# Kernel optimization log

Hardware: AMD Instinct MI355X
Metric: run time of the kernel (lower is better)

The kernel has to match this reference:

```python
import jax, jax.numpy as jnp
import numpy as np

K = 1024       # vq_codebook_size
DC = 64        # vq_code_dim
BETA = 0.25    # commitment cost
DECAY = 0.99   # EMA decay
EPS = 1e-05


def setup_inputs() -> dict:
    key = jax.random.key(0)
    k1, k2, k3 = jax.random.split(key, 3)
    B, H, W = 32, 64, 64
    return {
        "z_e": jax.random.normal(k1, (B, DC, H, W), dtype=jnp.float32),
        "embedding": jax.random.normal(k2, (K, DC), dtype=jnp.float32),
        "cluster_size": jnp.ones((K,), dtype=jnp.float32),
        "embed_avg": jax.random.normal(k3, (K, DC), dtype=jnp.float32),
    }


def reference(z_e, embedding, cluster_size, embed_avg):
    B, D, H, W = z_e.shape
    # flat: [N, D] detached codes, N = B*H*W
    flat = jax.lax.stop_gradient(z_e).transpose(0, 2, 3, 1).reshape(-1, D).astype(jnp.float32)
    distances = ((flat ** 2).sum(1, keepdims=True)
                 + (embedding ** 2).sum(1)
                 - 2.0 * flat @ embedding.T)
    indices = jnp.argmin(distances, axis=-1)          # [N]
    z_q_flat = embedding[indices]                      # gather [N, D]

    # EMA statistics (training path): one-hot sums via segment_sum (scatter-add)
    counts = jax.ops.segment_sum(jnp.ones_like(indices, dtype=jnp.float32), indices, num_segments=K)
    dw = jax.ops.segment_sum(flat, indices, num_segments=K)  # encodings.T @ flat
    new_cluster_size = cluster_size * DECAY + (1.0 - DECAY) * counts
    new_embed_avg = embed_avg * DECAY + (1.0 - DECAY) * dw
    n = new_cluster_size.sum()
    smoothed = (new_cluster_size + EPS) / (n + K * EPS) * n
    new_embedding = new_embed_avg / smoothed[:, None]

    z_q = z_q_flat.reshape(B, H, W, D).transpose(0, 3, 1, 2)  # [B, D, H, W]
    commitment_loss = BETA * jnp.mean((z_e.astype(jnp.float32) - jax.lax.stop_gradient(z_q)) ** 2)
    # straight-through estimator
    z_q_st = z_e + jax.lax.stop_gradient(z_q.astype(z_e.dtype) - z_e)
    return (z_q_st, indices.reshape(B, H, W), commitment_loss,
            new_embedding, new_cluster_size, new_embed_avg)
```

## Files before the change

kernel.cpp:

```cpp
#include <hip/hip_runtime.h>

#define KCB   1024
#define DCV   64
#define HWN   4096
#define CHW   262144
#define NTOT  131072

#define O_ZQ   0
#define O_IDX  8388608
#define O_LOSS 8519680
#define O_NE   8519681
#define O_NCS  8585217
#define O_NEA  8586241

#define W_LOSS  0
#define W_CTR   64
#define W_E2    256
#define W_HIT   8448
#define W_LOT   139520
#define W_EMBT  270592
#define W_RLIST 532736

#define RCAP   65536
#define MARGIN 0.01f

typedef __attribute__((ext_vector_type(8))) short short8v;
typedef __attribute__((ext_vector_type(4))) float f32x4;

__device__ __forceinline__ unsigned short rne16(float f) {
    unsigned u = __float_as_uint(f);
    unsigned r = (u + 0x7FFFu + ((u >> 16) & 1u)) >> 16;
    return (unsigned short)r;
}

__global__ __launch_bounds__(256) void k_init(
    const float* __restrict__ emb, const float* __restrict__ ea,
    const float* __restrict__ cs, float* __restrict__ out,
    float* __restrict__ e2, short* __restrict__ hiT, short* __restrict__ loT,
    float* __restrict__ embT, double* __restrict__ loss, int* __restrict__ ctr)
{
    int j = blockIdx.x * 256 + threadIdx.x;
    out[O_NEA + j] = 0.99f * ea[j];

    {
        int code = j >> 6, d = j & 63;
        embT[d * KCB + code] = emb[j];
    }
    if (j < KCB) {
        out[O_NCS + j] = 0.99f * cs[j];
        const float* er = emb + j * DCV;
        float s = 0.f;
        #pragma unroll
        for (int d = 0; d < DCV; ++d) { float v = er[d]; s = fmaf(v, v, s); }
        e2[j] = s;
    }
    if (j < 8192) {
        int code = j >> 3, q = j & 7;
        const float* src = emb + code * DCV + q * 8;
        short8v h, l;
        #pragma unroll
        for (int t = 0; t < 8; ++t) {
            float x = src[t];
            unsigned short hb = rne16(x);
            float xh = __uint_as_float(((unsigned)hb) << 16);
            h[t] = (short)hb;
            l[t] = (short)rne16(x - xh);
        }
        *(short8v*)(hiT + (size_t)(q * KCB + code) * 8) = h;
        *(short8v*)(loT + (size_t)(q * KCB + code) * 8) = l;
    }
    if (j == 0) { *loss = 0.0; *ctr = 0; }
}

__global__ __launch_bounds__(256, 2) void k_dist(
    const float* __restrict__ ze, const short* __restrict__ hiT,
    const short* __restrict__ loT, const float* __restrict__ e2g,
    float* __restrict__ out, int* __restrict__ ctr, int* __restrict__ rlist)
{
    __shared__ short ldsH[8 * 128 * 8];
    __shared__ short ldsL[8 * 128 * 8];
    __shared__ float e2s[KCB];

    int tid  = threadIdx.x;
    int lane = tid & 63, w = tid >> 6;
    int g = lane >> 4, c = lane & 15;

    for (int i = tid; i < KCB; i += 256) e2s[i] = e2g[i];

    int rowbase = blockIdx.x * 128 + w * 32;
    short8v ahi[2][2], alo[2][2];
    #pragma unroll
    for (int t = 0; t < 2; ++t) {
        int n = rowbase + t * 16 + c;
        const float* base = ze + (size_t)(n >> 12) * CHW + (n & 4095);
        #pragma unroll
        for (int kh = 0; kh < 2; ++kh) {
            #pragma unroll
            for (int j = 0; j < 8; ++j) {
                int k = kh * 32 + g * 8 + j;
                float x = base[(size_t)k * HWN];
                unsigned short hb = rne16(x);
                float xh = __uint_as_float(((unsigned)hb) << 16);
                ahi[t][kh][j] = (short)hb;
                alo[t][kh][j] = (short)rne16(x - xh);
            }
        }
    }

    float best[8], second[8];
    int   bidx[8];
    #pragma unroll
    for (int i = 0; i < 8; ++i) { best[i] = 3.4e38f; second[i] = 3.4e38f; bidx[i] = 0; }

    for (int ch = 0; ch < 8; ++ch) {
        __syncthreads();
        #pragma unroll
        for (int r = 0; r < 8; ++r) {
            int u = r * 256 + tid;
            int arr = u >> 10;
            int rest = u & 1023;
            int q = rest >> 7, lc = rest & 127;
            const short* s = (arr ? loT : hiT) + (size_t)(q * KCB + ch * 128 + lc) * 8;
            short* d = (arr ? ldsL : ldsH) + rest * 8;
            *(short8v*)d = *(const short8v*)s;
        }
        __syncthreads();

        #pragma unroll 1
        for (int sub = 0; sub < 8; ++sub) {
            int boff = (sub * 16 + c) * 8;
            short8v bh0 = *(const short8v*)&ldsH[(g * 128) * 8 + boff];
            short8v bh1 = *(const short8v*)&ldsH[((4 + g) * 128) * 8 + boff];
            short8v bl0 = *(const short8v*)&ldsL[(g * 128) * 8 + boff];
            short8v bl1 = *(const short8v*)&ldsL[((4 + g) * 128) * 8 + boff];

            f32x4 a0 = {0.f, 0.f, 0.f, 0.f}, a1 = {0.f, 0.f, 0.f, 0.f};
            a0 = __builtin_amdgcn_mfma_f32_16x16x32_bf16(ahi[0][0], bh0, a0, 0, 0, 0);
            a1 = __builtin_amdgcn_mfma_f32_16x16x32_bf16(ahi[1][0], bh0, a1, 0, 0, 0);
            a0 = __builtin_amdgcn_mfma_f32_16x16x32_bf16(ahi[0][1], bh1, a0, 0, 0, 0);
            a1 = __builtin_amdgcn_mfma_f32_16x16x32_bf16(ahi[1][1], bh1, a1, 0, 0, 0);
            a0 = __builtin_amdgcn_mfma_f32_16x16x32_bf16(ahi[0][0], bl0, a0, 0, 0, 0);
            a1 = __builtin_amdgcn_mfma_f32_16x16x32_bf16(ahi[1][0], bl0, a1, 0, 0, 0);
            a0 = __builtin_amdgcn_mfma_f32_16x16x32_bf16(ahi[0][1], bl1, a0, 0, 0, 0);
            a1 = __builtin_amdgcn_mfma_f32_16x16x32_bf16(ahi[1][1], bl1, a1, 0, 0, 0);
            a0 = __builtin_amdgcn_mfma_f32_16x16x32_bf16(alo[0][0], bh0, a0, 0, 0, 0);
            a1 = __builtin_amdgcn_mfma_f32_16x16x32_bf16(alo[1][0], bh0, a1, 0, 0, 0);
            a0 = __builtin_amdgcn_mfma_f32_16x16x32_bf16(alo[0][1], bh1, a0, 0, 0, 0);
            a1 = __builtin_amdgcn_mfma_f32_16x16x32_bf16(alo[1][1], bh1, a1, 0, 0, 0);

            float e2v = e2s[ch * 128 + sub * 16 + c];
            int  code = ch * 128 + sub * 16 + c;
            #pragma unroll
            for (int t = 0; t < 2; ++t) {
                f32x4 av = t ? a1 : a0;
                #pragma unroll
                for (int r = 0; r < 4; ++r) {
                    int i = t * 4 + r;
                    float s = fmaf(-2.f, av[r], e2v);
                    bool lb = s < best[i];
                    float m = lb ? best[i] : s;
                    second[i] = fminf(second[i], m);
                    best[i]   = fminf(best[i], s);
                    bidx[i]   = lb ? code : bidx[i];
                }
            }
        }
    }

    #pragma unroll
    for (int i = 0; i < 8; ++i) {
        float b = best[i], s2 = second[i];
        int bi = bidx[i];
        #pragma unroll
        for (int m = 1; m < 16; m <<= 1) {
            float ob = __shfl_xor(b, m, 64);
            float os = __shfl_xor(s2, m, 64);
            int   oi = __shfl_xor(bi, m, 64);
            float ns = fminf(fmaxf(b, ob), fminf(s2, os));
            bi = (ob < b || (ob == b && oi < bi)) ? oi : bi;
            b  = fminf(b, ob);
            s2 = ns;
        }
        if (c == 0) {
            int t = i >> 2, r = i & 3;
            int n = rowbase + t * 16 + g * 4 + r;
            out[O_IDX + n] = (float)bi;
            if (s2 - b < MARGIN) {
                int p = atomicAdd(ctr, 1);
                if (p < RCAP) rlist[p] = n;
            }
        }
    }
}

__global__ __launch_bounds__(256) void k_refine(
    const float* __restrict__ ze, const float* __restrict__ emb,
    float* __restrict__ out, const int* __restrict__ ctr,
    const int* __restrict__ rlist)
{
    int lane = threadIdx.x & 63;
    int gw   = (blockIdx.x * blockDim.x + threadIdx.x) >> 6;
    int nw   = (gridDim.x * blockDim.x) >> 6;
    int cnt  = *ctr;
    if (cnt > RCAP) cnt = RCAP;

    for (int i = gw; i < cnt; i += nw) {
        int n = rlist[i];
        const float* zp = ze + (size_t)(n >> 12) * CHW + (n & 4095);
        float x[DCV];
        #pragma unroll
        for (int d = 0; d < DCV; ++d) x[d] = zp[(size_t)d * HWN];

        double bd = 1e300;
        int    bi = 0;
        #pragma unroll 1
        for (int cc = 0; cc < KCB / 64; ++cc) {
            int k = cc * 64 + lane;
            const float4* eb4 = (const float4*)(emb + k * DCV);
            double a0 = 0.0, a1 = 0.0;
            #pragma unroll
            for (int q = 0; q < DCV / 4; ++q) {
                float4 v = eb4[q];
                double d0 = (double)x[q * 4 + 0] - (double)v.x;
                double d1 = (double)x[q * 4 + 1] - (double)v.y;
                double d2 = (double)x[q * 4 + 2] - (double)v.z;
                double d3 = (double)x[q * 4 + 3] - (double)v.w;
                a0 = fma(d0, d0, a0); a1 = fma(d1, d1, a1);
                a0 = fma(d2, d2, a0); a1 = fma(d3, d3, a1);
            }
            double dist = a0 + a1;
            if (dist < bd || (dist == bd && k < bi)) { bd = dist; bi = k; }
        }
        #pragma unroll
        for (int off = 32; off > 0; off >>= 1) {
            double od = __shfl_xor(bd, off, 64);
            int    oi = __shfl_xor(bi, off, 64);
            if (od < bd || (od == bd && oi < bi)) { bd = od; bi = oi; }
        }
        if (lane == 0) out[O_IDX + n] = (float)bi;
    }
}

__global__ __launch_bounds__(256) void k_post(
    const float* __restrict__ ze, const float* __restrict__ embT,
    float* __restrict__ out, double* __restrict__ loss)
{
    int gidx = blockIdx.x >> 5, b = blockIdx.x & 31;
    __shared__ float acc[8 * KCB];
    __shared__ float cnt[KCB];
    __shared__ float wsum[4];
    for (int i = threadIdx.x; i < 8 * KCB; i += 256) acc[i] = 0.f;
    if (gidx == 0) for (int i = threadIdx.x; i < KCB; i += 256) cnt[i] = 0.f;
    __syncthreads();

    const float* zp  = ze  + (size_t)b * CHW + (size_t)gidx * 8 * HWN;
    float*       zq  = out + O_ZQ + (size_t)b * CHW + (size_t)gidx * 8 * HWN;
    const float* ipf = out + O_IDX + b * HWN;
    const float* eT  = embT + (size_t)gidx * 8 * KCB;

    float lp = 0.f;
    for (int hw = threadIdx.x; hw < HWN; hw += 256) {
        int idx = (int)ipf[hw];
        #pragma unroll
        for (int i = 0; i < 8; ++i) {
            float x = zp[(size_t)i * HWN + hw];
            float e = eT[i * KCB + idx];
            float df = x - e;
            lp = fmaf(df, df, lp);
            zq[(size_t)i * HWN + hw] = x + (e - x);
            atomicAdd(&acc[idx * 8 + i], x);
        }
        if (gidx == 0) atomicAdd(&cnt[idx], 1.f);
    }

    #pragma unroll
    for (int off = 32; off > 0; off >>= 1) lp += __shfl_down(lp, off, 64);
    int lane = threadIdx.x & 63, wid = threadIdx.x >> 6;
    if (lane == 0) wsum[wid] = lp;
    __syncthreads();
    if (threadIdx.x == 0) {
        double s = (double)wsum[0] + wsum[1] + wsum[2] + wsum[3];
        atomicAdd(loss, s);
    }

    for (int j = threadIdx.x; j < 8192; j += 256) {
        float v = acc[j];
        if (v != 0.f) atomicAdd(&out[O_NEA + (j >> 3) * DCV + gidx * 8 + (j & 7)], 0.01f * v);
    }
    if (gidx == 0)
        for (int k = threadIdx.x; k < KCB; k += 256) {
            float cv = cnt[k];
            if (cv != 0.f) atomicAdd(&out[O_NCS + k], 0.01f * cv);
        }
}

__global__ __launch_bounds__(256) void k_fin(
    float* __restrict__ out, const double* __restrict__ loss)
{
    __shared__ float red[4];
    int t = threadIdx.x;
    float s = 0.f;
    #pragma unroll
    for (int q = 0; q < 4; ++q) s += out[O_NCS + t * 4 + q];
    #pragma unroll
    for (int off = 32; off > 0; off >>= 1) s += __shfl_down(s, off, 64);
    int lane = t & 63, wid = t >> 6;
    if (lane == 0) red[wid] = s;
    __syncthreads();
    float n = red[0] + red[1] + red[2] + red[3];

    int j = blockIdx.x * 256 + t;
    int k = j >> 6;
    float ncs = out[O_NCS + k];
    float sm = (ncs + 1e-5f) / (n + (float)KCB * 1e-5f) * n;
    out[O_NE + j] = out[O_NEA + j] / sm;

    if (blockIdx.x == 0 && t == 0)
        out[O_LOSS] = (float)(0.25 * (*loss) / (double)(NTOT * DCV));
}

extern "C" void kernel_launch(void* const* d_in, const int* in_sizes, int n_in,
                              void* d_out, int out_size, void* d_ws, size_t ws_size,
                              hipStream_t stream)
{
    const float* ze  = (const float*)d_in[0];
    const float* emb = (const float*)d_in[1];
    const float* cs  = (const float*)d_in[2];
    const float* ea  = (const float*)d_in[3];
    float* out = (float*)d_out;

    char*   w     = (char*)d_ws;
    double* loss  = (double*)(w + W_LOSS);
    int*    ctr   = (int*)(w + W_CTR);
    float*  e2    = (float*)(w + W_E2);
    short*  hiT   = (short*)(w + W_HIT);
    short*  loT   = (short*)(w + W_LOT);
    float*  embT  = (float*)(w + W_EMBT);
    int*    rlist = (int*)(w + W_RLIST);

    k_init  <<<256, 256, 0, stream>>>(emb, ea, cs, out, e2, hiT, loT, embT, loss, ctr);
    k_dist  <<<1024, 256, 0, stream>>>(ze, hiT, loT, e2, out, ctr, rlist);
    k_refine<<<256, 256, 0, stream>>>(ze, emb, out, ctr, rlist);
    k_post  <<<256, 256, 0, stream>>>(ze, embT, out, loss);
    k_fin   <<<256, 256, 0, stream>>>(out, loss);
}
```

Baseline: 247.6 us.

## Double-buffer codebook tiles via direct global-to-LDS loads with chunk-contiguous layout

Re-lays out the bf16 hi/lo codebook split so each 64-code chunk is contiguous, then stages chunks straight into LDS with global_load_lds into two alternating buffers. The next chunk's load overlaps the MFMA distance work on the current one, replacing the old synchronous load-then-compute loop that had two barriers per chunk. It also halves the ambiguity margin that sends rows to the exact fp32 refine pass, so fewer rows get refined. This adds more barrier iterations with smaller chunks, and the tighter margin raises the risk that a near-tie gets the wrong argmin.

Result: faster. 238.4 us (-3.7%).

```diff
diff --git a/kernel.cpp b/kernel.cpp
--- a/kernel.cpp
+++ b/kernel.cpp
@@ -16,13 +16,12 @@
 #define W_LOSS  0
 #define W_CTR   64
 #define W_E2    256
-#define W_HIT   8448
-#define W_LOT   139520
-#define W_EMBT  270592
-#define W_RLIST 532736
+#define W_HLT   4352
+#define W_EMBT  266496
+#define W_RLIST 528640
 
 #define RCAP   65536
-#define MARGIN 0.01f
+#define MARGIN 0.005f
 
 typedef __attribute__((ext_vector_type(8))) short short8v;
 typedef __attribute__((ext_vector_type(4))) float f32x4;
@@ -36,7 +35,7 @@
 __global__ __launch_bounds__(256) void k_init(
     const float* __restrict__ emb, const float* __restrict__ ea,
     const float* __restrict__ cs, float* __restrict__ out,
-    float* __restrict__ e2, short* __restrict__ hiT, short* __restrict__ loT,
+    float* __restrict__ e2, short* __restrict__ hl,
     float* __restrict__ embT, double* __restrict__ loss, int* __restrict__ ctr)
 {
     int j = blockIdx.x * 256 + threadIdx.x;
@@ -56,6 +55,7 @@
     }
     if (j < 8192) {
         int code = j >> 3, q = j & 7;
+        int ch = code >> 6, lc = code & 63;
         const float* src = emb + code * DCV + q * 8;
         short8v h, l;
         #pragma unroll
@@ -66,19 +66,18 @@
             h[t] = (short)hb;
             l[t] = (short)rne16(x - xh);
         }
-        *(short8v*)(hiT + (size_t)(q * KCB + code) * 8) = h;
-        *(short8v*)(loT + (size_t)(q * KCB + code) * 8) = l;
+        *(short8v*)(hl + (size_t)(((ch * 2 + 0) * 8 + q) * 64 + lc) * 8) = h;
+        *(short8v*)(hl + (size_t)(((ch * 2 + 1) * 8 + q) * 64 + lc) * 8) = l;
     }
     if (j == 0) { *loss = 0.0; *ctr = 0; }
 }
 
 __global__ __launch_bounds__(256, 2) void k_dist(
-    const float* __restrict__ ze, const short* __restrict__ hiT,
-    const short* __restrict__ loT, const float* __restrict__ e2g,
-    float* __restrict__ out, int* __restrict__ ctr, int* __restrict__ rlist)
-{
-    __shared__ short ldsH[8 * 128 * 8];
-    __shared__ short ldsL[8 * 128 * 8];
+    const float* __restrict__ ze, const char* __restrict__ hl,
+    const float* __restrict__ e2g, float* __restrict__ out,
+    int* __restrict__ ctr, int* __restrict__ rlist)
+{
+    __shared__ short lds[2][8192];
     __shared__ float e2s[KCB];
 
     int tid  = threadIdx.x;
@@ -86,6 +85,20 @@
     int g = lane >> 4, c = lane & 15;
 
     for (int i = tid; i < KCB; i += 256) e2s[i] = e2g[i];
+
+    #define STAGE(buf, ch)                                                     \
+        {                                                                      \
+            _Pragma("unroll")                                                  \
+            for (int r = 0; r < 4; ++r) {                                      \
+                int off = (r * 4 + w) * 1024 + lane * 16;                      \
+                __builtin_amdgcn_global_load_lds(                              \
+                    (const __attribute__((address_space(1))) void*)            \
+                        (hl + (size_t)(ch) * 16384 + off),                     \
+                    (__attribute__((address_space(3))) void*)                  \
+                        ((char*)lds[buf] + off),                               \
+                    16, 0, 0);                                                 \
+            }                                                                  \
+        }
 
     int rowbase = blockIdx.x * 128 + w * 32;
     short8v ahi[2][2], alo[2][2];
@@ -112,27 +125,21 @@
     #pragma unroll
     for (int i = 0; i < 8; ++i) { best[i] = 3.4e38f; second[i] = 3.4e38f; bidx[i] = 0; }
 
-    for (int ch = 0; ch < 8; ++ch) {
-        __syncthreads();
-        #pragma unroll
-        for (int r = 0; r < 8; ++r) {
-            int u = r * 256 + tid;
-            int arr = u >> 10;
-            int rest = u & 1023;
-            int q = rest >> 7, lc = rest & 127;
-            const short* s = (arr ? loT : hiT) + (size_t)(q * KCB + ch * 128 + lc) * 8;
-            short* d = (arr ? ldsL : ldsH) + rest * 8;
-            *(short8v*)d = *(const short8v*)s;
-        }
-        __syncthreads();
-
-        #pragma unroll 1
-        for (int sub = 0; sub < 8; ++sub) {
+    STAGE(0, 0);
+    __syncthreads();
+
+    int cur = 0;
+    for (int ch = 0; ch < 16; ++ch) {
+        if (ch < 15) STAGE(cur ^ 1, ch + 1);
+
+        const short* L = lds[cur];
+        #pragma unroll
+        for (int sub = 0; sub < 4; ++sub) {
             int boff = (sub * 16 + c) * 8;
-            short8v bh0 = *(const short8v*)&ldsH[(g * 128) * 8 + boff];
-            short8v bh1 = *(const short8v*)&ldsH[((4 + g) * 128) * 8 + boff];
-            short8v bl0 = *(const short8v*)&ldsL[(g * 128) * 8 + boff];
-            short8v bl1 = *(const short8v*)&ldsL[((4 + g) * 128) * 8 + boff];
+            short8v bh0 = *(const short8v*)&L[(g * 64) * 8 + boff];
+            short8v bh1 = *(const short8v*)&L[((4 + g) * 64) * 8 + boff];
+            short8v bl0 = *(const short8v*)&L[((8 + g) * 64) * 8 + boff];
+            short8v bl1 = *(const short8v*)&L[((12 + g) * 64) * 8 + boff];
 
             f32x4 a0 = {0.f, 0.f, 0.f, 0.f}, a1 = {0.f, 0.f, 0.f, 0.f};
             a0 = __builtin_amdgcn_mfma_f32_16x16x32_bf16(ahi[0][0], bh0, a0, 0, 0, 0);
@@ -148,8 +155,8 @@
             a0 = __builtin_amdgcn_mfma_f32_16x16x32_bf16(alo[0][1], bh1, a0, 0, 0, 0);
             a1 = __builtin_amdgcn_mfma_f32_16x16x32_bf16(alo[1][1], bh1, a1, 0, 0, 0);
 
-            float e2v = e2s[ch * 128 + sub * 16 + c];
-            int  code = ch * 128 + sub * 16 + c;
+            float e2v = e2s[ch * 64 + sub * 16 + c];
+            int  code = ch * 64 + sub * 16 + c;
             #pragma unroll
             for (int t = 0; t < 2; ++t) {
                 f32x4 av = t ? a1 : a0;
@@ -158,13 +165,14 @@
                     int i = t * 4 + r;
                     float s = fmaf(-2.f, av[r], e2v);
                     bool lb = s < best[i];
-                    float m = lb ? best[i] : s;
-                    second[i] = fminf(second[i], m);
+                    second[i] = fminf(second[i], fmaxf(best[i], s));
                     best[i]   = fminf(best[i], s);
                     bidx[i]   = lb ? code : bidx[i];
                 }
             }
         }
+        __syncthreads();
+        cur ^= 1;
     }
 
     #pragma unroll
@@ -191,6 +199,7 @@
             }
         }
     }
+    #undef STAGE
 }
 
 __global__ __launch_bounds__(256) void k_refine(
@@ -333,13 +342,12 @@
     double* loss  = (double*)(w + W_LOSS);
     int*    ctr   = (int*)(w + W_CTR);
     float*  e2    = (float*)(w + W_E2);
-    short*  hiT   = (short*)(w + W_HIT);
-    short*  loT   = (short*)(w + W_LOT);
+    short*  hl    = (short*)(w + W_HLT);
     float*  embT  = (float*)(w + W_EMBT);
     int*    rlist = (int*)(w + W_RLIST);
 
-    k_init  <<<256, 256, 0, stream>>>(emb, ea, cs, out, e2, hiT, loT, embT, loss, ctr);
-    k_dist  <<<1024, 256, 0, stream>>>(ze, hiT, loT, e2, out, ctr, rlist);
+    k_init  <<<256, 256, 0, stream>>>(emb, ea, cs, out, e2, hl, embT, loss, ctr);
+    k_dist  <<<1024, 256, 0, stream>>>(ze, (const char*)hl, e2, out, ctr, rlist);
     k_refine<<<256, 256, 0, stream>>>(ze, emb, out, ctr, rlist);
     k_post  <<<256, 256, 0, stream>>>(ze, embT, out, loss);
     k_fin   <<<256, 256, 0, stream>>>(out, loss);
```
